# Kernel optimization log

Measured on AMD Instinct MI355X. Metric: run time of the kernel, lower is better.

## Reference

```python
import jax, jax.numpy as jnp
import numpy as np

B, N, H, L = 8, 256, 128, 3
NF, EF, TD, FH = 6, 15, 4, 64  # node feat, edge feat, temporal dim, flow hidden


def setup_inputs() -> dict:
    key = jax.random.key(0)
    ks = jax.random.split(key, 16)
    s = 0.05
    return {
        "node_features": jax.random.normal(ks[0], (B, N, NF), jnp.float32),
        "edge_features": jax.random.normal(ks[1], (B, N, N, EF), jnp.float32),
        "temporal_features": jax.random.normal(ks[2], (B, N, N, TD), jnp.float32),
        "adjacency": jax.random.randint(ks[3], (N, N), 0, 2, jnp.int32),
        "W_emb": jax.random.normal(ks[4], (NF, H), jnp.float32) * s,
        "b_emb": jnp.zeros((H,), jnp.float32),
        "msg_W": jax.random.normal(ks[5], (L, H + 3, H), jnp.float32) * s,
        "msg_b": jnp.zeros((L, H), jnp.float32),
        "upd_W": jax.random.normal(ks[6], (L, 2 * H, H), jnp.float32) * s,
        "upd_b": jnp.zeros((L, H), jnp.float32),
        "W1": jax.random.normal(ks[7], (2 * H + 3 + TD, FH), jnp.float32) * s,
        "b1": jnp.zeros((FH,), jnp.float32),
        "W2": jax.random.normal(ks[8], (FH, 1), jnp.float32) * s,
        "b2": jnp.zeros((1,), jnp.float32),
    }


def reference(node_features, edge_features, temporal_features, adjacency,
              W_emb, b_emb, msg_W, msg_b, upd_W, upd_b, W1, b1, W2, b2):
    # mask[j, i] = 1 if node i is a neighbor of node j (adjacency[j] > 0)
    mask = (adjacency > 0).astype(node_features.dtype)          # [N, N]
    deg = mask.sum(axis=1)                                      # [N]
    edge_rel = edge_features[..., -3:]                          # [B, N, N, 3]
    # aggregated relation features per destination j: sum_i mask[j,i] * edge_rel[b,i,j,:]
    r_agg = jnp.einsum('ji,bijc->bjc', mask, edge_rel)          # [B, N, 3]

    # node embedding (dropout = identity in eval)
    emb = jax.nn.relu(node_features @ W_emb + b_emb)            # [B, N, H]

    for l in range(L):
        We, Wr = msg_W[l, :H], msg_W[l, H:]                     # [H,H], [3,H]
        # msg_nn is linear, so the masked sum decomposes exactly:
        # messages[b,j] = sum_i mask[j,i]*(emb_i @ We + r_ij @ Wr + b)
        messages = (jnp.einsum('ji,bih->bjh', mask, emb @ We)
                    + r_agg @ Wr
                    + deg[None, :, None] * msg_b[l])            # [B, N, H]
        emb = jax.nn.relu(
            jnp.concatenate([emb, messages], axis=-1) @ upd_W[l] + upd_b[l])

    # pairwise flow MLP, first Linear split by input blocks [emb_i, emb_j, r, t]
    Wi, Wj = W1[:H], W1[H:2 * H]
    Wr1, Wt = W1[2 * H:2 * H + 3], W1[2 * H + 3:]
    hi = emb @ Wi                                               # [B, N, FH]
    hj = emb @ Wj                                               # [B, N, FH]
    h = jax.nn.relu(hi[:, :, None, :] + hj[:, None, :, :]
                    + edge_rel @ Wr1 + temporal_features @ Wt + b1)  # [B,N,N,FH]
    flows = jax.nn.relu(h @ W2 + b2)[..., 0]                    # [B, N, N]
    return flows
```

## Files before the change

kernel.cpp:

```cpp
#include <hip/hip_runtime.h>

#define B 8
#define N 256
#define H 128
#define NF 6
#define EF 15
#define TD 4
#define FH 64
#define M (B*N)

typedef unsigned short u16;
using short8  = __attribute__((ext_vector_type(8))) short;
using short4v = __attribute__((ext_vector_type(4))) short;
using f32x4   = __attribute__((ext_vector_type(4))) float;

__device__ __forceinline__ u16 f2bf(float x) {
    unsigned u = __float_as_uint(x);
    u += 0x7fffu + ((u >> 16) & 1u);
    return (u16)(u >> 16);
}
__device__ __forceinline__ float bf2f(u16 h) {
    return __uint_as_float(((unsigned)h) << 16);
}

#define PIPE(NC, LD, COMP)                          \
    LD(0, pA0, pA1);                                \
    LD(1, pB0, pB1);                                \
    WRX(0, pA0, pA1);                               \
    __syncthreads();                                \
    _Pragma("unroll")                               \
    for (int c = 0; c < (NC); c += 2) {             \
        WRX(1, pB0, pB1);                           \
        if (c + 2 < (NC)) LD(c + 2, pA0, pA1);      \
        COMP(c, 0);                                 \
        __syncthreads();                            \
        if (c + 2 < (NC)) WRX(0, pA0, pA1);         \
        if (c + 3 < (NC)) LD(c + 3, pB0, pB1);      \
        COMP(c + 1, 1);                             \
        __syncthreads();                            \
    }

__global__ __launch_bounds__(256) void k_setup(
    const float* __restrict__ edge, const int* __restrict__ adj,
    const float* __restrict__ nf, const float* __restrict__ Wemb,
    const float* __restrict__ bemb,
    const float* __restrict__ msg_W, const float* __restrict__ upd_W,
    const float* __restrict__ W1,
    float* __restrict__ e0p, float* __restrict__ e1p, float* __restrict__ e2p,
    float* __restrict__ rp0, float* __restrict__ rp1, float* __restrict__ rp2,
    float* __restrict__ deg,
    u16* __restrict__ WeTh, u16* __restrict__ WeTl,
    u16* __restrict__ UwTh, u16* __restrict__ UwTl,
    u16* __restrict__ W1Th, u16* __restrict__ W1Tl,
    u16* __restrict__ eRh, u16* __restrict__ eRl,
    u16* __restrict__ eTh, u16* __restrict__ eTl)
{
    __shared__ __align__(16) float smem[3848];
    __shared__ float red[4];
    const int t = threadIdx.x;
    const int blk = blockIdx.x;

    if (blk < 2048) {
        const int i = blk & 255;
        const float* src = edge + (size_t)blk * (N * EF);
        float4* s4 = (float4*)smem;
#pragma unroll
        for (int u = 0; u < 4; ++u) {
            int idx = t + u * 256;
            if (idx < (N * EF) / 4) s4[idx] = *(const float4*)(src + idx * 4);
        }
        __syncthreads();
        const int j = t;
        float e0 = smem[j * EF + 12];
        float e1 = smem[j * EF + 13];
        float e2 = smem[j * EF + 14];
        size_t base = (size_t)blk * N + j;
        e0p[base] = e0; e1p[base] = e1; e2p[base] = e2;
        float m = (adj[j * N + i] > 0) ? 1.f : 0.f;
        rp0[base] = m * e0; rp1[base] = m * e1; rp2[base] = m * e2;
    } else if (blk < 2688) {
        int idx = (blk - 2048) * 256 + t;
        float v; u16 *dh, *dl; int d;
        if (idx < 3 * 16384) {
            int l = idx / 16384, r = idx & 16383;
            int c = r >> 7, h = r & 127;
            v = msg_W[l * ((H + 3) * H) + h * H + c];
            dh = WeTh; dl = WeTl; d = idx;
        } else if (idx < 3 * 16384 + 3 * 32768) {
            int r0 = idx - 3 * 16384;
            int l = r0 / 32768, r = r0 & 32767;
            int c = r >> 8, k = r & 255;
            v = upd_W[l * (2 * H * H) + k * H + c];
            dh = UwTh; dl = UwTl; d = r0;
        } else {
            int r0 = idx - 3 * 16384 - 3 * 32768;
            int f = r0 >> 8, k = r0 & 255;
            v = W1[k * FH + f];
            dh = W1Th; dl = W1Tl; d = r0;
        }
        u16 h = f2bf(v);
        dh[d] = h;
        dl[d] = f2bf(v - bf2f(h));
    } else if (blk < 2816) {
        int tile = blk - 2688;
        float (*sout)[132] = (float(*)[132])smem;
        {
            int row = t >> 4, h0 = (t & 15) * 8;
            int gr = tile * 16 + row;
            float xv[NF];
#pragma unroll
            for (int k = 0; k < NF; ++k) xv[k] = nf[gr * NF + k];
#pragma unroll
            for (int c = 0; c < 8; ++c) {
                float a = bemb[h0 + c];
#pragma unroll
                for (int k = 0; k < NF; ++k) a += xv[k] * Wemb[k * H + h0 + c];
                sout[row][h0 + c] = fmaxf(a, 0.f);
            }
        }
        __syncthreads();
        {
            int row = t >> 4, h0 = (t & 15) * 8;
            int gr = tile * 16 + row;
            short8 ph, pl;
#pragma unroll
            for (int c = 0; c < 8; ++c) {
                float x = sout[row][h0 + c];
                u16 h = f2bf(x);
                ph[c] = (short)h;
                pl[c] = (short)f2bf(x - bf2f(h));
            }
            *(short8*)&eRh[(size_t)gr * H + h0] = ph;
            *(short8*)&eRl[(size_t)gr * H + h0] = pl;
        }
        {
            int hh = t >> 1, jj = (t & 1) * 8;
            short8 th, tl;
#pragma unroll
            for (int r = 0; r < 8; ++r) {
                float x = sout[jj + r][hh];
                u16 h = f2bf(x);
                th[r] = (short)h;
                tl[r] = (short)f2bf(x - bf2f(h));
            }
            size_t o = (size_t)(tile >> 4) * H * N + (size_t)hh * N + ((tile & 15) * 16) + jj;
            *(short8*)&eTh[o] = th;
            *(short8*)&eTl[o] = tl;
        }
    } else {
        int jr = blk - 2816;
        float v = (adj[jr * N + t] > 0) ? 1.f : 0.f;
        for (int o = 32; o > 0; o >>= 1) v += __shfl_down(v, o);
        if ((t & 63) == 0) red[t >> 6] = v;
        __syncthreads();
        if (t == 0) deg[jr] = red[0] + red[1] + red[2] + red[3];
    }
}

template <bool FIRST, bool LAST>
__global__ __launch_bounds__(512) void k_layer(
    const u16* __restrict__ embR_hi, const u16* __restrict__ embR_lo,
    const u16* __restrict__ embT_hi, const u16* __restrict__ embT_lo,
    const int* __restrict__ adj,
    const float* __restrict__ rp0, const float* __restrict__ rp1,
    const float* __restrict__ rp2, float* __restrict__ ragg,
    const float* __restrict__ deg,
    const u16* __restrict__ WeT_hi, const u16* __restrict__ WeT_lo,
    const float* __restrict__ mwl, const float* __restrict__ mbl,
    const u16* __restrict__ UwT_hi, const u16* __restrict__ UwT_lo,
    const float* __restrict__ ubl,
    u16* __restrict__ oR_hi, u16* __restrict__ oR_lo,
    u16* __restrict__ oT_hi, u16* __restrict__ oT_lo,
    const u16* __restrict__ W1T_hi, const u16* __restrict__ W1T_lo,
    float* __restrict__ hi_out, float* __restrict__ hj_out)
{
    __shared__ __align__(16) u16 sbt[2][2][128][40];
    __shared__ __align__(16) u16 smask[16][264];
    __shared__ __align__(16) u16 semb_hi[16][136], semb_lo[16][136];
    __shared__ __align__(16) u16 sagg_hi[16][136], sagg_lo[16][136];
    __shared__ __align__(16) u16 smsg_hi[16][136], smsg_lo[16][136];
    __shared__ __align__(16) float sout[16][132];
    __shared__ float sragg[16][4];

    const int t = threadIdx.x;
    const int wave = t >> 6, lane = t & 63;
    const int lrow = lane & 15;
    const int kg8  = (lane >> 4) * 8;
    const int rb   = (lane >> 4) * 4;
    const int cb   = wave * 16;
    const int blk  = blockIdx.x;
    const int b    = blk >> 4, tile = blk & 15;
    const int j0   = tile * 16;
    const int gb   = b * N;

    const int sp = t >> 8, task = t & 255;
    const int sh = task >> 2, sseg = (task & 3) * 8;

    short8 pA0, pA1, pB0, pB1;

    {
        int j = t >> 5, i0 = (t & 31) * 8;
        int4 a0 = *(const int4*)(adj + (j0 + j) * N + i0);
        int4 a1 = *(const int4*)(adj + (j0 + j) * N + i0 + 4);
        short8 mrow;
        mrow[0] = (a0.x > 0) ? (short)0x3F80 : (short)0;
        mrow[1] = (a0.y > 0) ? (short)0x3F80 : (short)0;
        mrow[2] = (a0.z > 0) ? (short)0x3F80 : (short)0;
        mrow[3] = (a0.w > 0) ? (short)0x3F80 : (short)0;
        mrow[4] = (a1.x > 0) ? (short)0x3F80 : (short)0;
        mrow[5] = (a1.y > 0) ? (short)0x3F80 : (short)0;
        mrow[6] = (a1.z > 0) ? (short)0x3F80 : (short)0;
        mrow[7] = (a1.w > 0) ? (short)0x3F80 : (short)0;
        *(short8*)&smask[j][i0] = mrow;
        int h0 = (t & 31) * 4;
        *(short4v*)&semb_hi[j][h0] = *(const short4v*)&embR_hi[(size_t)(gb + j0 + j) * H + h0];
        *(short4v*)&semb_lo[j][h0] = *(const short4v*)&embR_lo[(size_t)(gb + j0 + j) * H + h0];
    }

    if constexpr (FIRST) {
        int j16 = t >> 5, ic = t & 31;
        int gj = gb + j0 + j16;
        float s0 = 0.f, s1 = 0.f, s2 = 0.f;
#pragma unroll
        for (int k = 0; k < 8; ++k) {
            size_t o = ((size_t)(gb + ic * 8 + k)) * N + (j0 + j16);
            s0 += rp0[o]; s1 += rp1[o]; s2 += rp2[o];
        }
        for (int o = 16; o > 0; o >>= 1) {
            s0 += __shfl_down(s0, o, 32);
            s1 += __shfl_down(s1, o, 32);
            s2 += __shfl_down(s2, o, 32);
        }
        if (ic == 0) {
            sragg[j16][0] = s0; sragg[j16][1] = s1; sragg[j16][2] = s2;
            float* rg = ragg + (size_t)gj * 3;
            rg[0] = s0; rg[1] = s1; rg[2] = s2;
        }
    } else {
        if (t < 48) sragg[t / 3][t % 3] = ragg[(size_t)(gb + j0 + t / 3) * 3 + (t % 3)];
    }

    const u16* sA_hi = embT_hi + (size_t)b * H * N;
    const u16* sA_lo = embT_lo + (size_t)b * H * N;

#define WRX(buf, q0, q1)                              \
    { *(short8*)&sbt[buf][sp][sh][sseg] = q0;         \
      *(short8*)&sbt[buf][sp][sh + 64][sseg] = q1; }

#define LDA(c, q0, q1)                                                        \
    { const u16* s_ = sp ? sA_lo : sA_hi;                                     \
      q0 = *(const short8*)(s_ + (size_t)sh * N + (c) * 32 + sseg);           \
      q1 = *(const short8*)(s_ + (size_t)(sh + 64) * N + (c) * 32 + sseg); }

#define LDB(c, q0, q1)                                                        \
    { const u16* s_ = sp ? WeT_lo : WeT_hi;                                   \
      q0 = *(const short8*)(s_ + (size_t)sh * H + (c) * 32 + sseg);           \
      q1 = *(const short8*)(s_ + (size_t)(sh + 64) * H + (c) * 32 + sseg); }

#define LDC(c, q0, q1)                                                        \
    { const u16* s_ = sp ? UwT_lo : UwT_hi;                                   \
      q0 = *(const short8*)(s_ + (size_t)sh * 2 * H + (c) * 32 + sseg);       \
      q1 = *(const short8*)(s_ + (size_t)(sh + 64) * 2 * H + (c) * 32 + sseg); }

#define LDD(c, q0, q1)                                                        \
    { const u16* s_ = sp ? W1T_lo : W1T_hi;                                   \
      q0 = *(const short8*)(s_ + (size_t)sh * 256 + (c) * 32 + sseg);         \
      q1 = *(const short8*)(s_ + (size_t)sh * 256 + 128 + (c) * 32 + sseg); }

#define COMPA(c, buf)                                                           \
    { short8 am = *(const short8*)&smask[lrow][(c) * 32 + kg8];                 \
      short8 bh = *(const short8*)&sbt[buf][0][cb + lrow][kg8];                 \
      short8 bl = *(const short8*)&sbt[buf][1][cb + lrow][kg8];                 \
      acc = __builtin_amdgcn_mfma_f32_16x16x32_bf16(am, bh, acc, 0, 0, 0);      \
      acc = __builtin_amdgcn_mfma_f32_16x16x32_bf16(am, bl, acc, 0, 0, 0); }

#define COMPB(c, buf)                                                           \
    { short8 ah = *(const short8*)&sagg_hi[lrow][(c) * 32 + kg8];               \
      short8 al = *(const short8*)&sagg_lo[lrow][(c) * 32 + kg8];               \
      short8 bh = *(const short8*)&sbt[buf][0][cb + lrow][kg8];                 \
      short8 bl = *(const short8*)&sbt[buf][1][cb + lrow][kg8];                 \
      acc = __builtin_amdgcn_mfma_f32_16x16x32_bf16(ah, bh, acc, 0, 0, 0);      \
      acc = __builtin_amdgcn_mfma_f32_16x16x32_bf16(ah, bl, acc, 0, 0, 0);      \
      acc = __builtin_amdgcn_mfma_f32_16x16x32_bf16(al, bh, acc, 0, 0, 0); }

#define COMPC(c, buf)                                                           \
    { int kc = ((c) & 3) * 32 + kg8; short8 ah, al;                             \
      if ((c) < 4) { ah = *(const short8*)&semb_hi[lrow][kc];                   \
                     al = *(const short8*)&semb_lo[lrow][kc]; }                 \
      else         { ah = *(const short8*)&smsg_hi[lrow][kc];                   \
                     al = *(const short8*)&smsg_lo[lrow][kc]; }                 \
      short8 bh = *(const short8*)&sbt[buf][0][cb + lrow][kg8];                 \
      short8 bl = *(const short8*)&sbt[buf][1][cb + lrow][kg8];                 \
      acc = __builtin_amdgcn_mfma_f32_16x16x32_bf16(ah, bh, acc, 0, 0, 0);      \
      acc = __builtin_amdgcn_mfma_f32_16x16x32_bf16(ah, bl, acc, 0, 0, 0);      \
      acc = __builtin_amdgcn_mfma_f32_16x16x32_bf16(al, bh, acc, 0, 0, 0); }

#define COMPD(c, buf)                                                           \
    { short8 ah = *(const short8*)&sagg_hi[lrow][(c) * 32 + kg8];               \
      short8 al = *(const short8*)&sagg_lo[lrow][(c) * 32 + kg8];               \
      short8 bh = *(const short8*)&sbt[buf][0][br][kg8];                        \
      short8 bl = *(const short8*)&sbt[buf][1][br][kg8];                        \
      acc = __builtin_amdgcn_mfma_f32_16x16x32_bf16(ah, bh, acc, 0, 0, 0);      \
      acc = __builtin_amdgcn_mfma_f32_16x16x32_bf16(ah, bl, acc, 0, 0, 0);      \
      acc = __builtin_amdgcn_mfma_f32_16x16x32_bf16(al, bh, acc, 0, 0, 0); }

    f32x4 acc = {0.f, 0.f, 0.f, 0.f};
    PIPE(8, LDA, COMPA)
#pragma unroll
    for (int r = 0; r < 4; ++r) {
        float v = acc[r];
        u16 h = f2bf(v);
        sagg_hi[rb + r][cb + lrow] = h;
        sagg_lo[rb + r][cb + lrow] = f2bf(v - bf2f(h));
    }

    acc = (f32x4){0.f, 0.f, 0.f, 0.f};
    PIPE(4, LDB, COMPB)
    {
        int hp = cb + lrow;
        float w0 = mwl[(H + 0) * H + hp];
        float w1 = mwl[(H + 1) * H + hp];
        float w2 = mwl[(H + 2) * H + hp];
        float mb = mbl[hp];
#pragma unroll
        for (int r = 0; r < 4; ++r) {
            int jl = j0 + rb + r;
            float v = acc[r] + deg[jl] * mb
                    + sragg[rb + r][0] * w0 + sragg[rb + r][1] * w1
                    + sragg[rb + r][2] * w2;
            u16 h = f2bf(v);
            smsg_hi[rb + r][hp] = h;
            smsg_lo[rb + r][hp] = f2bf(v - bf2f(h));
        }
    }

    acc = (f32x4){0.f, 0.f, 0.f, 0.f};
    PIPE(8, LDC, COMPC)
    {
        float ub = ubl[cb + lrow];
#pragma unroll
        for (int r = 0; r < 4; ++r) {
            float v = fmaxf(acc[r] + ub, 0.f);
            if constexpr (LAST) {
                u16 h = f2bf(v);
                sagg_hi[rb + r][cb + lrow] = h;
                sagg_lo[rb + r][cb + lrow] = f2bf(v - bf2f(h));
            } else {
                sout[rb + r][cb + lrow] = v;
            }
        }
    }
    __syncthreads();

    if constexpr (!LAST) {
        {
            int row = t >> 5, h0 = (t & 31) * 4;
            int gr = gb + j0 + row;
            float4 v = *(const float4*)&sout[row][h0];
            float xs[4] = {v.x, v.y, v.z, v.w};
            short4v ph, pl;
#pragma unroll
            for (int c = 0; c < 4; ++c) {
                u16 h = f2bf(xs[c]);
                ph[c] = (short)h;
                pl[c] = (short)f2bf(xs[c] - bf2f(h));
            }
            *(short4v*)&oR_hi[(size_t)gr * H + h0] = ph;
            *(short4v*)&oR_lo[(size_t)gr * H + h0] = pl;
        }
        {
            int hh = t >> 2, jj = (t & 3) * 4;
            short4v th, tl;
#pragma unroll
            for (int r = 0; r < 4; ++r) {
                float x = sout[jj + r][hh];
                u16 h = f2bf(x);
                th[r] = (short)h;
                tl[r] = (short)f2bf(x - bf2f(h));
            }
            size_t o = (size_t)b * H * N + (size_t)hh * N + j0 + jj;
            *(short4v*)&oT_hi[o] = th;
            *(short4v*)&oT_lo[o] = tl;
        }
    } else {
        const int br = ((wave >= 4) ? 64 : 0) + (wave & 3) * 16 + lrow;
        acc = (f32x4){0.f, 0.f, 0.f, 0.f};
        PIPE(4, LDD, COMPD)
#pragma unroll
        for (int r = 0; r < 4; ++r) sout[rb + r][br] = acc[r];
        __syncthreads();
        int row = t >> 5, c0 = (t & 31) * 4;
        int gr = gb + j0 + row;
        float4 v = *(const float4*)&sout[row][c0];
        if (c0 < 64) *(float4*)&hi_out[(size_t)gr * FH + c0] = v;
        else         *(float4*)&hj_out[(size_t)gr * FH + (c0 - 64)] = v;
    }
#undef WRX
#undef LDA
#undef LDB
#undef LDC
#undef LDD
#undef COMPA
#undef COMPB
#undef COMPC
#undef COMPD
}

__global__ __launch_bounds__(256) void k_final(
    const float* __restrict__ hi, const float* __restrict__ hj,
    const float* __restrict__ e0p, const float* __restrict__ e1p,
    const float* __restrict__ e2p, const float* __restrict__ temporal,
    const float* __restrict__ W1, const float* __restrict__ b1,
    const float* __restrict__ W2, const float* __restrict__ b2,
    float* __restrict__ flows) {
    __shared__ __align__(16) float his[8][FH];
    __shared__ __align__(16) float hjs[32][FH + 4];
    int blk = blockIdx.x;
    int jt = blk & 7, it = (blk >> 3) & 31, b = blk >> 8;
    int tid = threadIdx.x;
#pragma unroll
    for (int u = 0; u < 2; ++u) {
        int idx = u * 256 + tid;
        his[idx >> 6][idx & 63] = hi[((size_t)(b * N) + it * 8 + (idx >> 6)) * FH + (idx & 63)];
    }
#pragma unroll
    for (int u = 0; u < 8; ++u) {
        int idx = u * 256 + tid;
        hjs[idx >> 6][idx & 63] = hj[((size_t)(b * N) + jt * 32 + (idx >> 6)) * FH + (idx & 63)];
    }
    __syncthreads();
    int ti = tid >> 5, tj = tid & 31;
    int i = it * 8 + ti, j = jt * 32 + tj;
    size_t pij = ((size_t)(b * N) + i) * N + j;
    float e0 = e0p[pij], e1 = e1p[pij], e2 = e2p[pij];
    float4 tf = *(const float4*)(temporal + pij * TD);
    const float* Wx = W1 + (2 * H) * FH;
    float acc = 0.f;
#pragma unroll
    for (int f0 = 0; f0 < FH; f0 += 4) {
        float4 h4 = *(const float4*)&his[ti][f0];
        float4 g4 = *(const float4*)&hjs[tj][f0];
        float4 r0 = *(const float4*)(Wx + 0 * FH + f0);
        float4 r1 = *(const float4*)(Wx + 1 * FH + f0);
        float4 r2 = *(const float4*)(Wx + 2 * FH + f0);
        float4 t0 = *(const float4*)(Wx + 3 * FH + f0);
        float4 t1 = *(const float4*)(Wx + 4 * FH + f0);
        float4 t2 = *(const float4*)(Wx + 5 * FH + f0);
        float4 t3 = *(const float4*)(Wx + 6 * FH + f0);
        float4 bb = *(const float4*)(b1 + f0);
        float4 w2 = *(const float4*)(W2 + f0);
        float v;
        v = h4.x + g4.x + bb.x + e0 * r0.x + e1 * r1.x + e2 * r2.x
          + tf.x * t0.x + tf.y * t1.x + tf.z * t2.x + tf.w * t3.x;
        acc += fmaxf(v, 0.f) * w2.x;
        v = h4.y + g4.y + bb.y + e0 * r0.y + e1 * r1.y + e2 * r2.y
          + tf.x * t0.y + tf.y * t1.y + tf.z * t2.y + tf.w * t3.y;
        acc += fmaxf(v, 0.f) * w2.y;
        v = h4.z + g4.z + bb.z + e0 * r0.z + e1 * r1.z + e2 * r2.z
          + tf.x * t0.z + tf.y * t1.z + tf.z * t2.z + tf.w * t3.z;
        acc += fmaxf(v, 0.f) * w2.z;
        v = h4.w + g4.w + bb.w + e0 * r0.w + e1 * r1.w + e2 * r2.w
          + tf.x * t0.w + tf.y * t1.w + tf.z * t2.w + tf.w * t3.w;
        acc += fmaxf(v, 0.f) * w2.w;
    }
    flows[pij] = fmaxf(acc + b2[0], 0.f);
}

extern "C" void kernel_launch(void* const* d_in, const int* in_sizes, int n_in,
                              void* d_out, int out_size, void* d_ws, size_t ws_size,
                              hipStream_t stream) {
    const float* nf       = (const float*)d_in[0];
    const float* edge     = (const float*)d_in[1];
    const float* temporal = (const float*)d_in[2];
    const int*   adj      = (const int*)d_in[3];
    const float* W_emb    = (const float*)d_in[4];
    const float* b_emb    = (const float*)d_in[5];
    const float* msg_W    = (const float*)d_in[6];
    const float* msg_b    = (const float*)d_in[7];
    const float* upd_W    = (const float*)d_in[8];
    const float* upd_b    = (const float*)d_in[9];
    const float* W1       = (const float*)d_in[10];
    const float* b1       = (const float*)d_in[11];
    const float* W2       = (const float*)d_in[12];
    const float* b2       = (const float*)d_in[13];
    float* out = (float*)d_out;
    (void)in_sizes; (void)n_in; (void)out_size; (void)ws_size;

    char* p = (char*)d_ws;
    auto take = [&](size_t bytes) { char* r = p; p += (bytes + 255) & ~(size_t)255; return r; };
    float* deg   = (float*)take(256 * 4);
    float* ragg  = (float*)take((size_t)M * 3 * 4);
    float* e0p   = (float*)take((size_t)B * N * N * 4);
    float* e1p   = (float*)take((size_t)B * N * N * 4);
    float* e2p   = (float*)take((size_t)B * N * N * 4);
    float* rp0   = (float*)take((size_t)B * N * N * 4);
    float* rp1   = (float*)take((size_t)B * N * N * 4);
    float* rp2   = (float*)take((size_t)B * N * N * 4);
    float* hi    = (float*)take((size_t)M * FH * 4);
    float* hj    = (float*)take((size_t)M * FH * 4);
    u16* eRhA = (u16*)take((size_t)M * H * 2);
    u16* eRlA = (u16*)take((size_t)M * H * 2);
    u16* eThA = (u16*)take((size_t)M * H * 2);
    u16* eTlA = (u16*)take((size_t)M * H * 2);
    u16* eRhB = (u16*)take((size_t)M * H * 2);
    u16* eRlB = (u16*)take((size_t)M * H * 2);
    u16* eThB = (u16*)take((size_t)M * H * 2);
    u16* eTlB = (u16*)take((size_t)M * H * 2);
    u16* WeTh = (u16*)take(3 * 16384 * 2);
    u16* WeTl = (u16*)take(3 * 16384 * 2);
    u16* UwTh = (u16*)take(3 * 32768 * 2);
    u16* UwTl = (u16*)take(3 * 32768 * 2);
    u16* W1Th = (u16*)take(16384 * 2);
    u16* W1Tl = (u16*)take(16384 * 2);

    k_setup<<<3072, 256, 0, stream>>>(edge, adj, nf, W_emb, b_emb,
                                      msg_W, upd_W, W1,
                                      e0p, e1p, e2p, rp0, rp1, rp2, deg,
                                      WeTh, WeTl, UwTh, UwTl, W1Th, W1Tl,
                                      eRhA, eRlA, eThA, eTlA);

    const int mwS = (H + 3) * H;
    k_layer<true, false><<<128, 512, 0, stream>>>(
        eRhA, eRlA, eThA, eTlA, adj, rp0, rp1, rp2, ragg, deg,
        WeTh + 0 * 16384, WeTl + 0 * 16384, msg_W + 0 * mwS, msg_b + 0 * H,
        UwTh + 0 * 32768, UwTl + 0 * 32768, upd_b + 0 * H,
        eRhB, eRlB, eThB, eTlB, W1Th, W1Tl, hi, hj);
    k_layer<false, false><<<128, 512, 0, stream>>>(
        eRhB, eRlB, eThB, eTlB, adj, rp0, rp1, rp2, ragg, deg,
        WeTh + 1 * 16384, WeTl + 1 * 16384, msg_W + 1 * mwS, msg_b + 1 * H,
        UwTh + 1 * 32768, UwTl + 1 * 32768, upd_b + 1 * H,
        eRhA, eRlA, eThA, eTlA, W1Th, W1Tl, hi, hj);
    k_layer<false, true><<<128, 512, 0, stream>>>(
        eRhA, eRlA, eThA, eTlA, adj, rp0, rp1, rp2, ragg, deg,
        WeTh + 2 * 16384, WeTl + 2 * 16384, msg_W + 2 * mwS, msg_b + 2 * H,
        UwTh + 2 * 32768, UwTl + 2 * 32768, upd_b + 2 * H,
        eRhB, eRlB, eThB, eTlB, W1Th, W1Tl, hi, hj);

    k_final<<<2048, 256, 0, stream>>>(hi, hj, e0p, e1p, e2p, temporal,
                                      W1, b1, W2, b2, out);
}
```

Before: 67.42 us.

## Atomically aggregate relation sums in setup, store edge slices as bf16, widen K chunks

The setup kernel no longer writes six full B*N*N float arrays. It accumulates the masked relation sums directly into ragg with atomics and stores the three edge channels as bf16, which cuts workspace traffic and removes the reduction pass from the first layer. The layer kernels double the K chunk per pipeline stage (64 instead of 32), halving barrier count at the cost of more registers and shared memory. The final kernel folds b1 into the staged hi values and splits the accumulator. Storing the edge channels as bf16 lowers precision, and float atomics make the summation order nondeterministic.

Result: slower. 109.1 us (+61.9%).

```diff
diff --git a/kernel.cpp b/kernel.cpp
--- a/kernel.cpp
+++ b/kernel.cpp
@@ -23,61 +23,38 @@
     return __uint_as_float(((unsigned)h) << 16);
 }
 
-#define PIPE(NC, LD, COMP)                          \
-    LD(0, pA0, pA1);                                \
-    LD(1, pB0, pB1);                                \
-    WRX(0, pA0, pA1);                               \
-    __syncthreads();                                \
-    _Pragma("unroll")                               \
-    for (int c = 0; c < (NC); c += 2) {             \
-        WRX(1, pB0, pB1);                           \
-        if (c + 2 < (NC)) LD(c + 2, pA0, pA1);      \
-        COMP(c, 0);                                 \
-        __syncthreads();                            \
-        if (c + 2 < (NC)) WRX(0, pA0, pA1);         \
-        if (c + 3 < (NC)) LD(c + 3, pB0, pB1);      \
-        COMP(c + 1, 1);                             \
-        __syncthreads();                            \
-    }
-
 __global__ __launch_bounds__(256) void k_setup(
     const float* __restrict__ edge, const int* __restrict__ adj,
     const float* __restrict__ nf, const float* __restrict__ Wemb,
     const float* __restrict__ bemb,
     const float* __restrict__ msg_W, const float* __restrict__ upd_W,
     const float* __restrict__ W1,
-    float* __restrict__ e0p, float* __restrict__ e1p, float* __restrict__ e2p,
-    float* __restrict__ rp0, float* __restrict__ rp1, float* __restrict__ rp2,
-    float* __restrict__ deg,
+    u16* __restrict__ e0p, u16* __restrict__ e1p, u16* __restrict__ e2p,
+    float* __restrict__ ragg, float* __restrict__ deg,
     u16* __restrict__ WeTh, u16* __restrict__ WeTl,
     u16* __restrict__ UwTh, u16* __restrict__ UwTl,
     u16* __restrict__ W1Th, u16* __restrict__ W1Tl,
     u16* __restrict__ eRh, u16* __restrict__ eRl,
     u16* __restrict__ eTh, u16* __restrict__ eTl)
 {
-    __shared__ __align__(16) float smem[3848];
+    __shared__ __align__(16) float smem[16][132];
     __shared__ float red[4];
     const int t = threadIdx.x;
     const int blk = blockIdx.x;
 
     if (blk < 2048) {
-        const int i = blk & 255;
-        const float* src = edge + (size_t)blk * (N * EF);
-        float4* s4 = (float4*)smem;
-#pragma unroll
-        for (int u = 0; u < 4; ++u) {
-            int idx = t + u * 256;
-            if (idx < (N * EF) / 4) s4[idx] = *(const float4*)(src + idx * 4);
-        }
-        __syncthreads();
+        const int b = blk >> 8, i = blk & 255;
         const int j = t;
-        float e0 = smem[j * EF + 12];
-        float e1 = smem[j * EF + 13];
-        float e2 = smem[j * EF + 14];
-        size_t base = (size_t)blk * N + j;
-        e0p[base] = e0; e1p[base] = e1; e2p[base] = e2;
-        float m = (adj[j * N + i] > 0) ? 1.f : 0.f;
-        rp0[base] = m * e0; rp1[base] = m * e1; rp2[base] = m * e2;
+        size_t rec = (size_t)blk * N + j;
+        const float* e = edge + rec * EF + (EF - 3);
+        float e0 = e[0], e1 = e[1], e2 = e[2];
+        e0p[rec] = f2bf(e0); e1p[rec] = f2bf(e1); e2p[rec] = f2bf(e2);
+        if (adj[j * N + i] > 0) {
+            float* rg = ragg + ((size_t)(b * N) + j) * 3;
+            atomicAdd(rg + 0, e0);
+            atomicAdd(rg + 1, e1);
+            atomicAdd(rg + 2, e2);
+        }
     } else if (blk < 2688) {
         int idx = (blk - 2048) * 256 + t;
         float v; u16 *dh, *dl; int d;
@@ -103,7 +80,6 @@
         dl[d] = f2bf(v - bf2f(h));
     } else if (blk < 2816) {
         int tile = blk - 2688;
-        float (*sout)[132] = (float(*)[132])smem;
         {
             int row = t >> 4, h0 = (t & 15) * 8;
             int gr = tile * 16 + row;
@@ -115,7 +91,7 @@
                 float a = bemb[h0 + c];
 #pragma unroll
                 for (int k = 0; k < NF; ++k) a += xv[k] * Wemb[k * H + h0 + c];
-                sout[row][h0 + c] = fmaxf(a, 0.f);
+                smem[row][h0 + c] = fmaxf(a, 0.f);
             }
         }
         __syncthreads();
@@ -125,7 +101,7 @@
             short8 ph, pl;
 #pragma unroll
             for (int c = 0; c < 8; ++c) {
-                float x = sout[row][h0 + c];
+                float x = smem[row][h0 + c];
                 u16 h = f2bf(x);
                 ph[c] = (short)h;
                 pl[c] = (short)f2bf(x - bf2f(h));
@@ -138,7 +114,7 @@
             short8 th, tl;
 #pragma unroll
             for (int r = 0; r < 8; ++r) {
-                float x = sout[jj + r][hh];
+                float x = smem[jj + r][hh];
                 u16 h = f2bf(x);
                 th[r] = (short)h;
                 tl[r] = (short)f2bf(x - bf2f(h));
@@ -157,13 +133,28 @@
     }
 }
 
-template <bool FIRST, bool LAST>
+#define PIPE2(NC, LDM, COMP)                                \
+    LDM(0, pA0, pA1, pA2, pA3);                             \
+    if ((NC) > 1) LDM(1, pB0, pB1, pB2, pB3);               \
+    WRX(0, pA0, pA1, pA2, pA3);                             \
+    __syncthreads();                                        \
+    _Pragma("unroll")                                       \
+    for (int c = 0; c < (NC); c += 2) {                     \
+        if (c + 1 < (NC)) WRX(1, pB0, pB1, pB2, pB3);       \
+        if (c + 2 < (NC)) LDM(c + 2, pA0, pA1, pA2, pA3);   \
+        COMP(c, 0);                                         \
+        __syncthreads();                                    \
+        if (c + 2 < (NC)) WRX(0, pA0, pA1, pA2, pA3);       \
+        if (c + 3 < (NC)) LDM(c + 3, pB0, pB1, pB2, pB3);   \
+        if (c + 1 < (NC)) COMP(c + 1, 1);                   \
+        __syncthreads();                                    \
+    }
+
+template <bool LAST>
 __global__ __launch_bounds__(512) void k_layer(
     const u16* __restrict__ embR_hi, const u16* __restrict__ embR_lo,
     const u16* __restrict__ embT_hi, const u16* __restrict__ embT_lo,
-    const int* __restrict__ adj,
-    const float* __restrict__ rp0, const float* __restrict__ rp1,
-    const float* __restrict__ rp2, float* __restrict__ ragg,
+    const int* __restrict__ adj, const float* __restrict__ ragg,
     const float* __restrict__ deg,
     const u16* __restrict__ WeT_hi, const u16* __restrict__ WeT_lo,
     const float* __restrict__ mwl, const float* __restrict__ mbl,
@@ -174,7 +165,7 @@
     const u16* __restrict__ W1T_hi, const u16* __restrict__ W1T_lo,
     float* __restrict__ hi_out, float* __restrict__ hj_out)
 {
-    __shared__ __align__(16) u16 sbt[2][2][128][40];
+    __shared__ __align__(16) u16 sbt[2][2][128][72];
     __shared__ __align__(16) u16 smask[16][264];
     __shared__ __align__(16) u16 semb_hi[16][136], semb_lo[16][136];
     __shared__ __align__(16) u16 sagg_hi[16][136], sagg_lo[16][136];
@@ -194,9 +185,9 @@
     const int gb   = b * N;
 
     const int sp = t >> 8, task = t & 255;
-    const int sh = task >> 2, sseg = (task & 3) * 8;
-
-    short8 pA0, pA1, pB0, pB1;
+    const int sh = task >> 2, sseg = (task & 3) * 16;
+
+    short8 pA0, pA1, pA2, pA3, pB0, pB1, pB2, pB3;
 
     {
         int j = t >> 5, i0 = (t & 31) * 8;
@@ -215,97 +206,98 @@
         int h0 = (t & 31) * 4;
         *(short4v*)&semb_hi[j][h0] = *(const short4v*)&embR_hi[(size_t)(gb + j0 + j) * H + h0];
         *(short4v*)&semb_lo[j][h0] = *(const short4v*)&embR_lo[(size_t)(gb + j0 + j) * H + h0];
-    }
-
-    if constexpr (FIRST) {
-        int j16 = t >> 5, ic = t & 31;
-        int gj = gb + j0 + j16;
-        float s0 = 0.f, s1 = 0.f, s2 = 0.f;
-#pragma unroll
-        for (int k = 0; k < 8; ++k) {
-            size_t o = ((size_t)(gb + ic * 8 + k)) * N + (j0 + j16);
-            s0 += rp0[o]; s1 += rp1[o]; s2 += rp2[o];
-        }
-        for (int o = 16; o > 0; o >>= 1) {
-            s0 += __shfl_down(s0, o, 32);
-            s1 += __shfl_down(s1, o, 32);
-            s2 += __shfl_down(s2, o, 32);
-        }
-        if (ic == 0) {
-            sragg[j16][0] = s0; sragg[j16][1] = s1; sragg[j16][2] = s2;
-            float* rg = ragg + (size_t)gj * 3;
-            rg[0] = s0; rg[1] = s1; rg[2] = s2;
-        }
-    } else {
         if (t < 48) sragg[t / 3][t % 3] = ragg[(size_t)(gb + j0 + t / 3) * 3 + (t % 3)];
     }
 
     const u16* sA_hi = embT_hi + (size_t)b * H * N;
     const u16* sA_lo = embT_lo + (size_t)b * H * N;
 
-#define WRX(buf, q0, q1)                              \
-    { *(short8*)&sbt[buf][sp][sh][sseg] = q0;         \
-      *(short8*)&sbt[buf][sp][sh + 64][sseg] = q1; }
-
-#define LDA(c, q0, q1)                                                        \
-    { const u16* s_ = sp ? sA_lo : sA_hi;                                     \
-      q0 = *(const short8*)(s_ + (size_t)sh * N + (c) * 32 + sseg);           \
-      q1 = *(const short8*)(s_ + (size_t)(sh + 64) * N + (c) * 32 + sseg); }
-
-#define LDB(c, q0, q1)                                                        \
-    { const u16* s_ = sp ? WeT_lo : WeT_hi;                                   \
-      q0 = *(const short8*)(s_ + (size_t)sh * H + (c) * 32 + sseg);           \
-      q1 = *(const short8*)(s_ + (size_t)(sh + 64) * H + (c) * 32 + sseg); }
-
-#define LDC(c, q0, q1)                                                        \
-    { const u16* s_ = sp ? UwT_lo : UwT_hi;                                   \
-      q0 = *(const short8*)(s_ + (size_t)sh * 2 * H + (c) * 32 + sseg);       \
-      q1 = *(const short8*)(s_ + (size_t)(sh + 64) * 2 * H + (c) * 32 + sseg); }
-
-#define LDD(c, q0, q1)                                                        \
-    { const u16* s_ = sp ? W1T_lo : W1T_hi;                                   \
-      q0 = *(const short8*)(s_ + (size_t)sh * 256 + (c) * 32 + sseg);         \
-      q1 = *(const short8*)(s_ + (size_t)sh * 256 + 128 + (c) * 32 + sseg); }
-
-#define COMPA(c, buf)                                                           \
-    { short8 am = *(const short8*)&smask[lrow][(c) * 32 + kg8];                 \
-      short8 bh = *(const short8*)&sbt[buf][0][cb + lrow][kg8];                 \
-      short8 bl = *(const short8*)&sbt[buf][1][cb + lrow][kg8];                 \
-      acc = __builtin_amdgcn_mfma_f32_16x16x32_bf16(am, bh, acc, 0, 0, 0);      \
-      acc = __builtin_amdgcn_mfma_f32_16x16x32_bf16(am, bl, acc, 0, 0, 0); }
-
-#define COMPB(c, buf)                                                           \
-    { short8 ah = *(const short8*)&sagg_hi[lrow][(c) * 32 + kg8];               \
-      short8 al = *(const short8*)&sagg_lo[lrow][(c) * 32 + kg8];               \
-      short8 bh = *(const short8*)&sbt[buf][0][cb + lrow][kg8];                 \
-      short8 bl = *(const short8*)&sbt[buf][1][cb + lrow][kg8];                 \
-      acc = __builtin_amdgcn_mfma_f32_16x16x32_bf16(ah, bh, acc, 0, 0, 0);      \
-      acc = __builtin_amdgcn_mfma_f32_16x16x32_bf16(ah, bl, acc, 0, 0, 0);      \
-      acc = __builtin_amdgcn_mfma_f32_16x16x32_bf16(al, bh, acc, 0, 0, 0); }
-
-#define COMPC(c, buf)                                                           \
-    { int kc = ((c) & 3) * 32 + kg8; short8 ah, al;                             \
-      if ((c) < 4) { ah = *(const short8*)&semb_hi[lrow][kc];                   \
-                     al = *(const short8*)&semb_lo[lrow][kc]; }                 \
-      else         { ah = *(const short8*)&smsg_hi[lrow][kc];                   \
-                     al = *(const short8*)&smsg_lo[lrow][kc]; }                 \
-      short8 bh = *(const short8*)&sbt[buf][0][cb + lrow][kg8];                 \
-      short8 bl = *(const short8*)&sbt[buf][1][cb + lrow][kg8];                 \
-      acc = __builtin_amdgcn_mfma_f32_16x16x32_bf16(ah, bh, acc, 0, 0, 0);      \
-      acc = __builtin_amdgcn_mfma_f32_16x16x32_bf16(ah, bl, acc, 0, 0, 0);      \
-      acc = __builtin_amdgcn_mfma_f32_16x16x32_bf16(al, bh, acc, 0, 0, 0); }
-
-#define COMPD(c, buf)                                                           \
-    { short8 ah = *(const short8*)&sagg_hi[lrow][(c) * 32 + kg8];               \
-      short8 al = *(const short8*)&sagg_lo[lrow][(c) * 32 + kg8];               \
-      short8 bh = *(const short8*)&sbt[buf][0][br][kg8];                        \
-      short8 bl = *(const short8*)&sbt[buf][1][br][kg8];                        \
-      acc = __builtin_amdgcn_mfma_f32_16x16x32_bf16(ah, bh, acc, 0, 0, 0);      \
-      acc = __builtin_amdgcn_mfma_f32_16x16x32_bf16(ah, bl, acc, 0, 0, 0);      \
-      acc = __builtin_amdgcn_mfma_f32_16x16x32_bf16(al, bh, acc, 0, 0, 0); }
+#define WRX(buf, q0, q1, q2, q3)                        \
+    { *(short8*)&sbt[buf][sp][sh][sseg] = q0;           \
+      *(short8*)&sbt[buf][sp][sh][sseg + 8] = q1;       \
+      *(short8*)&sbt[buf][sp][sh + 64][sseg] = q2;      \
+      *(short8*)&sbt[buf][sp][sh + 64][sseg + 8] = q3; }
+
+#define LDA(c, q0, q1, q2, q3)                                                  \
+    { const u16* s_ = sp ? sA_lo : sA_hi;                                       \
+      q0 = *(const short8*)(s_ + (size_t)sh * N + (c) * 64 + sseg);             \
+      q1 = *(const short8*)(s_ + (size_t)sh * N + (c) * 64 + sseg + 8);         \
+      q2 = *(const short8*)(s_ + (size_t)(sh + 64) * N + (c) * 64 + sseg);      \
+      q3 = *(const short8*)(s_ + (size_t)(sh + 64) * N + (c) * 64 + sseg + 8); }
+
+#define LDB(c, q0, q1, q2, q3)                                                  \
+    { const u16* s_ = sp ? WeT_lo : WeT_hi;                                     \
+      q0 = *(const short8*)(s_ + (size_t)sh * H + (c) * 64 + sseg);             \
+      q1 = *(const short8*)(s_ + (size_t)sh * H + (c) * 64 + sseg + 8);         \
+      q2 = *(const short8*)(s_ + (size_t)(sh + 64) * H + (c) * 64 + sseg);      \
+      q3 = *(const short8*)(s_ + (size_t)(sh + 64) * H + (c) * 64 + sseg + 8); }
+
+#define LDC(c, q0, q1, q2, q3)                                                      \
+    { const u16* s_ = sp ? UwT_lo : UwT_hi;                                         \
+      q0 = *(const short8*)(s_ + (size_t)sh * 2 * H + (c) * 64 + sseg);             \
+      q1 = *(const short8*)(s_ + (size_t)sh * 2 * H + (c) * 64 + sseg + 8);         \
+      q2 = *(const short8*)(s_ + (size_t)(sh + 64) * 2 * H + (c) * 64 + sseg);      \
+      q3 = *(const short8*)(s_ + (size_t)(sh + 64) * 2 * H + (c) * 64 + sseg + 8); }
+
+#define LDD(c, q0, q1, q2, q3)                                                  \
+    { const u16* s_ = sp ? W1T_lo : W1T_hi;                                     \
+      q0 = *(const short8*)(s_ + (size_t)sh * 256 + (c) * 64 + sseg);           \
+      q1 = *(const short8*)(s_ + (size_t)sh * 256 + (c) * 64 + sseg + 8);       \
+      q2 = *(const short8*)(s_ + (size_t)sh * 256 + 128 + (c) * 64 + sseg);     \
+      q3 = *(const short8*)(s_ + (size_t)sh * 256 + 128 + (c) * 64 + sseg + 8); }
+
+#define COMPA(c, buf)                                                               \
+    _Pragma("unroll")                                                               \
+    for (int ks = 0; ks < 2; ++ks) {                                                \
+        short8 am = *(const short8*)&smask[lrow][(c) * 64 + ks * 32 + kg8];         \
+        short8 bh = *(const short8*)&sbt[buf][0][cb + lrow][ks * 32 + kg8];         \
+        short8 bl = *(const short8*)&sbt[buf][1][cb + lrow][ks * 32 + kg8];         \
+        acc = __builtin_amdgcn_mfma_f32_16x16x32_bf16(am, bh, acc, 0, 0, 0);        \
+        acc = __builtin_amdgcn_mfma_f32_16x16x32_bf16(am, bl, acc, 0, 0, 0);        \
+    }
+
+#define COMPB(c, buf)                                                               \
+    _Pragma("unroll")                                                               \
+    for (int ks = 0; ks < 2; ++ks) {                                                \
+        short8 ah = *(const short8*)&sagg_hi[lrow][(c) * 64 + ks * 32 + kg8];       \
+        short8 al = *(const short8*)&sagg_lo[lrow][(c) * 64 + ks * 32 + kg8];       \
+        short8 bh = *(const short8*)&sbt[buf][0][cb + lrow][ks * 32 + kg8];         \
+        short8 bl = *(const short8*)&sbt[buf][1][cb + lrow][ks * 32 + kg8];         \
+        acc = __builtin_amdgcn_mfma_f32_16x16x32_bf16(ah, bh, acc, 0, 0, 0);        \
+        acc = __builtin_amdgcn_mfma_f32_16x16x32_bf16(ah, bl, acc, 0, 0, 0);        \
+        acc = __builtin_amdgcn_mfma_f32_16x16x32_bf16(al, bh, acc, 0, 0, 0);        \
+    }
+
+#define COMPC(c, buf)                                                               \
+    _Pragma("unroll")                                                               \
+    for (int ks = 0; ks < 2; ++ks) {                                                \
+        int kc = ((c) & 1) * 64 + ks * 32 + kg8;                                    \
+        short8 ah, al;                                                              \
+        if ((c) < 2) { ah = *(const short8*)&semb_hi[lrow][kc];                     \
+                       al = *(const short8*)&semb_lo[lrow][kc]; }                   \
+        else         { ah = *(const short8*)&smsg_hi[lrow][kc];                     \
+                       al = *(const short8*)&smsg_lo[lrow][kc]; }                   \
+        short8 bh = *(const short8*)&sbt[buf][0][cb + lrow][ks * 32 + kg8];         \
+        short8 bl = *(const short8*)&sbt[buf][1][cb + lrow][ks * 32 + kg8];         \
+        acc = __builtin_amdgcn_mfma_f32_16x16x32_bf16(ah, bh, acc, 0, 0, 0);        \
+        acc = __builtin_amdgcn_mfma_f32_16x16x32_bf16(ah, bl, acc, 0, 0, 0);        \
+        acc = __builtin_amdgcn_mfma_f32_16x16x32_bf16(al, bh, acc, 0, 0, 0);        \
+    }
+
+#define COMPD(c, buf)                                                               \
+    _Pragma("unroll")                                                               \
+    for (int ks = 0; ks < 2; ++ks) {                                                \
+        short8 ah = *(const short8*)&sagg_hi[lrow][(c) * 64 + ks * 32 + kg8];       \
+        short8 al = *(const short8*)&sagg_lo[lrow][(c) * 64 + ks * 32 + kg8];       \
+        short8 bh = *(const short8*)&sbt[buf][0][br][ks * 32 + kg8];                \
+        short8 bl = *(const short8*)&sbt[buf][1][br][ks * 32 + kg8];                \
+        acc = __builtin_amdgcn_mfma_f32_16x16x32_bf16(ah, bh, acc, 0, 0, 0);        \
+        acc = __builtin_amdgcn_mfma_f32_16x16x32_bf16(ah, bl, acc, 0, 0, 0);        \
+        acc = __builtin_amdgcn_mfma_f32_16x16x32_bf16(al, bh, acc, 0, 0, 0);        \
+    }
 
     f32x4 acc = {0.f, 0.f, 0.f, 0.f};
-    PIPE(8, LDA, COMPA)
+    PIPE2(4, LDA, COMPA)
 #pragma unroll
     for (int r = 0; r < 4; ++r) {
         float v = acc[r];
@@ -315,7 +307,7 @@
     }
 
     acc = (f32x4){0.f, 0.f, 0.f, 0.f};
-    PIPE(4, LDB, COMPB)
+    PIPE2(2, LDB, COMPB)
     {
         int hp = cb + lrow;
         float w0 = mwl[(H + 0) * H + hp];
@@ -335,7 +327,7 @@
     }
 
     acc = (f32x4){0.f, 0.f, 0.f, 0.f};
-    PIPE(8, LDC, COMPC)
+    PIPE2(4, LDC, COMPC)
     {
         float ub = ubl[cb + lrow];
 #pragma unroll
@@ -385,7 +377,7 @@
     } else {
         const int br = ((wave >= 4) ? 64 : 0) + (wave & 3) * 16 + lrow;
         acc = (f32x4){0.f, 0.f, 0.f, 0.f};
-        PIPE(4, LDD, COMPD)
+        PIPE2(2, LDD, COMPD)
 #pragma unroll
         for (int r = 0; r < 4; ++r) sout[rb + r][br] = acc[r];
         __syncthreads();
@@ -408,8 +400,8 @@
 
 __global__ __launch_bounds__(256) void k_final(
     const float* __restrict__ hi, const float* __restrict__ hj,
-    const float* __restrict__ e0p, const float* __restrict__ e1p,
-    const float* __restrict__ e2p, const float* __restrict__ temporal,
+    const u16* __restrict__ e0p, const u16* __restrict__ e1p,
+    const u16* __restrict__ e2p, const float* __restrict__ temporal,
     const float* __restrict__ W1, const float* __restrict__ b1,
     const float* __restrict__ W2, const float* __restrict__ b2,
     float* __restrict__ flows) {
@@ -421,7 +413,8 @@
 #pragma unroll
     for (int u = 0; u < 2; ++u) {
         int idx = u * 256 + tid;
-        his[idx >> 6][idx & 63] = hi[((size_t)(b * N) + it * 8 + (idx >> 6)) * FH + (idx & 63)];
+        his[idx >> 6][idx & 63] =
+            hi[((size_t)(b * N) + it * 8 + (idx >> 6)) * FH + (idx & 63)] + b1[idx & 63];
     }
 #pragma unroll
     for (int u = 0; u < 8; ++u) {
@@ -432,10 +425,10 @@
     int ti = tid >> 5, tj = tid & 31;
     int i = it * 8 + ti, j = jt * 32 + tj;
     size_t pij = ((size_t)(b * N) + i) * N + j;
-    float e0 = e0p[pij], e1 = e1p[pij], e2 = e2p[pij];
+    float e0 = bf2f(e0p[pij]), e1 = bf2f(e1p[pij]), e2 = bf2f(e2p[pij]);
     float4 tf = *(const float4*)(temporal + pij * TD);
     const float* Wx = W1 + (2 * H) * FH;
-    float acc = 0.f;
+    float accA = 0.f, accB = 0.f;
 #pragma unroll
     for (int f0 = 0; f0 < FH; f0 += 4) {
         float4 h4 = *(const float4*)&his[ti][f0];
@@ -447,23 +440,22 @@
         float4 t1 = *(const float4*)(Wx + 4 * FH + f0);
         float4 t2 = *(const float4*)(Wx + 5 * FH + f0);
         float4 t3 = *(const float4*)(Wx + 6 * FH + f0);
-        float4 bb = *(const float4*)(b1 + f0);
         float4 w2 = *(const float4*)(W2 + f0);
         float v;
-        v = h4.x + g4.x + bb.x + e0 * r0.x + e1 * r1.x + e2 * r2.x
+        v = h4.x + g4.x + e0 * r0.x + e1 * r1.x + e2 * r2.x
           + tf.x * t0.x + tf.y * t1.x + tf.z * t2.x + tf.w * t3.x;
-        acc += fmaxf(v, 0.f) * w2.x;
-        v = h4.y + g4.y + bb.y + e0 * r0.y + e1 * r1.y + e2 * r2.y
+        accA += fmaxf(v, 0.f) * w2.x;
+        v = h4.y + g4.y + e0 * r0.y + e1 * r1.y + e2 * r2.y
           + tf.x * t0.y + tf.y * t1.y + tf.z * t2.y + tf.w * t3.y;
-        acc += fmaxf(v, 0.f) * w2.y;
-        v = h4.z + g4.z + bb.z + e0 * r0.z + e1 * r1.z + e2 * r2.z
+        accB += fmaxf(v, 0.f) * w2.y;
+        v = h4.z + g4.z + e0 * r0.z + e1 * r1.z + e2 * r2.z
           + tf.x * t0.z + tf.y * t1.z + tf.z * t2.z + tf.w * t3.z;
-        acc += fmaxf(v, 0.f) * w2.z;
-        v = h4.w + g4.w + bb.w + e0 * r0.w + e1 * r1.w + e2 * r2.w
+        accA += fmaxf(v, 0.f) * w2.z;
+        v = h4.w + g4.w + e0 * r0.w + e1 * r1.w + e2 * r2.w
           + tf.x * t0.w + tf.y * t1.w + tf.z * t2.w + tf.w * t3.w;
-        acc += fmaxf(v, 0.f) * w2.w;
-    }
-    flows[pij] = fmaxf(acc + b2[0], 0.f);
+        accB += fmaxf(v, 0.f) * w2.w;
+    }
+    flows[pij] = fmaxf(accA + accB + b2[0], 0.f);
 }
 
 extern "C" void kernel_launch(void* const* d_in, const int* in_sizes, int n_in,
@@ -490,12 +482,9 @@
     auto take = [&](size_t bytes) { char* r = p; p += (bytes + 255) & ~(size_t)255; return r; };
     float* deg   = (float*)take(256 * 4);
     float* ragg  = (float*)take((size_t)M * 3 * 4);
-    float* e0p   = (float*)take((size_t)B * N * N * 4);
-    float* e1p   = (float*)take((size_t)B * N * N * 4);
-    float* e2p   = (float*)take((size_t)B * N * N * 4);
-    float* rp0   = (float*)take((size_t)B * N * N * 4);
-    float* rp1   = (float*)take((size_t)B * N * N * 4);
-    float* rp2   = (float*)take((size_t)B * N * N * 4);
+    u16* e0p     = (u16*)take((size_t)B * N * N * 2);
+    u16* e1p     = (u16*)take((size_t)B * N * N * 2);
+    u16* e2p     = (u16*)take((size_t)B * N * N * 2);
     float* hi    = (float*)take((size_t)M * FH * 4);
     float* hj    = (float*)take((size_t)M * FH * 4);
     u16* eRhA = (u16*)take((size_t)M * H * 2);
@@ -513,25 +502,27 @@
     u16* W1Th = (u16*)take(16384 * 2);
     u16* W1Tl = (u16*)take(16384 * 2);
 
+    hipMemsetAsync(ragg, 0, (size_t)M * 3 * 4, stream);
+
     k_setup<<<3072, 256, 0, stream>>>(edge, adj, nf, W_emb, b_emb,
                                       msg_W, upd_W, W1,
-                                      e0p, e1p, e2p, rp0, rp1, rp2, deg,
+                                      e0p, e1p, e2p, ragg, deg,
                                       WeTh, WeTl, UwTh, UwTl, W1Th, W1Tl,
                                       eRhA, eRlA, eThA, eTlA);
 
     const int mwS = (H + 3) * H;
-    k_layer<true, false><<<128, 512, 0, stream>>>(
-        eRhA, eRlA, eThA, eTlA, adj, rp0, rp1, rp2, ragg, deg,
+    k_layer<false><<<128, 512, 0, stream>>>(
+        eRhA, eRlA, eThA, eTlA, adj, ragg, deg,
         WeTh + 0 * 16384, WeTl + 0 * 16384, msg_W + 0 * mwS, msg_b + 0 * H,
         UwTh + 0 * 32768, UwTl + 0 * 32768, upd_b + 0 * H,
         eRhB, eRlB, eThB, eTlB, W1Th, W1Tl, hi, hj);
-    k_layer<false, false><<<128, 512, 0, stream>>>(
-        eRhB, eRlB, eThB, eTlB, adj, rp0, rp1, rp2, ragg, deg,
+    k_layer<false><<<128, 512, 0, stream>>>(
+        eRhB, eRlB, eThB, eTlB, adj, ragg, deg,
         WeTh + 1 * 16384, WeTl + 1 * 16384, msg_W + 1 * mwS, msg_b + 1 * H,
         UwTh + 1 * 32768, UwTl + 1 * 32768, upd_b + 1 * H,
         eRhA, eRlA, eThA, eTlA, W1Th, W1Tl, hi, hj);
-    k_layer<false, true><<<128, 512, 0, stream>>>(
-        eRhA, eRlA, eThA, eTlA, adj, rp0, rp1, rp2, ragg, deg,
+    k_layer<true><<<128, 512, 0, stream>>>(
+        eRhA, eRlA, eThA, eTlA, adj, ragg, deg,
         WeTh + 2 * 16384, WeTl + 2 * 16384, msg_W + 2 * mwS, msg_b + 2 * H,
         UwTh + 2 * 32768, UwTl + 2 * 32768, upd_b + 2 * H,
         eRhB, eRlB, eThB, eTlB, W1Th, W1Tl, hi, hj);
```
